# Performance work log

Measured on AMD Instinct MI355X. Metric: run time of the kernel, lower is better.

The kernel has to match this reference:

```python
import jax, jax.numpy as jnp
import numpy as np

LEAK = 0.95
THRESHOLD = 1.0
CLAMP = 3.0
LN_EPS = 1e-5


def setup_inputs() -> dict:
    key = jax.random.key(0)
    k1, k2 = jax.random.split(key)
    B, S, V, D = 8, 2048, 57344, 1536
    token_ids = jax.random.randint(k1, (B, S), 0, V, dtype=jnp.int64)
    emb_table = jax.random.normal(k2, (V, D), dtype=jnp.float32) * 0.02
    gamma = jnp.ones((D,), dtype=jnp.float32)
    beta = jnp.zeros((D,), dtype=jnp.float32)
    return {"token_ids": token_ids, "emb_table": emb_table, "gamma": gamma, "beta": beta}


def _layernorm(x, gamma, beta):
    mu = jnp.mean(x, axis=-1, keepdims=True)
    var = jnp.mean(jnp.square(x - mu), axis=-1, keepdims=True)
    return (x - mu) * jax.lax.rsqrt(var + LN_EPS) * gamma + beta


def _lif_scan(x):
    # x: [B, S, D]; sequential LIF recurrence over time axis S
    B, S, D = x.shape
    v0 = jnp.zeros((B, D), dtype=x.dtype)

    def step(v, xt):
        v = v * LEAK + xt
        v = jnp.clip(v, -CLAMP, CLAMP)
        spike = (v >= THRESHOLD).astype(x.dtype)
        return v * (1.0 - spike), spike

    _, spikes = jax.lax.scan(step, v0, jnp.swapaxes(x, 0, 1))  # spikes: [S, B, D]
    return jnp.swapaxes(spikes, 0, 1)


def reference(token_ids, emb_table, gamma, beta):
    x = emb_table[token_ids]          # [B, S, D] embedding lookup
    x = _layernorm(x, gamma, beta)    # continuous residual stream
    spikes = _lif_scan(x)             # 0/1 spike tensor [B, S, D]
    return spikes, x
```

## Files before the change

kernel.cpp:

```cpp
#include <hip/hip_runtime.h>


constexpr int Bv = 8, Sv = 2048, Dv = 1536;
constexpr int Cn = 32;
constexpr int Ln = Sv / Cn;
constexpr int Wn = 64;
constexpr int BD = Bv * Dv;
constexpr int TNMAX = Ln + Wn;

constexpr size_t FLAG_OFF  = 0;
constexpr size_t STATS_OFF = 64;
constexpr size_t SPEC0_OFF = STATS_OFF + (size_t)2 * Bv * Sv * 8;
constexpr size_t SPEC1_OFF = SPEC0_OFF + (size_t)Cn * BD * 8;
constexpr size_t WS_NEED   = SPEC1_OFF + (size_t)Cn * BD * 8;

__device__ __forceinline__ double ln_x64(float e, double mu, double rs,
                                         double gd, double bd) {
#pragma clang fp contract(off)
    return (((double)e - mu) * rs) * gd + bd;
}
__device__ __forceinline__ double lif_step(double v, double x, bool& spike) {
#pragma clang fp contract(off)
    double vv = v * 0.95;
    vv = vv + x;
    vv = fmin(fmax(vv, -3.0), 3.0);
    spike = (vv >= 1.0);
    return spike ? 0.0 : vv;
}

extern "C" __global__ __launch_bounds__(1024)
void detect_tok64(const int* __restrict__ tok, int* __restrict__ flag)
{
    __shared__ int any_nz;
    if (threadIdx.x == 0) any_nz = 0;
    __syncthreads();
    int nz = 0;
    for (int i = threadIdx.x; i < (Bv * Sv) / 2; i += 1024) nz |= tok[2 * i + 1];
    if (nz) atomicOr(&any_nz, 1);
    __syncthreads();
    if (threadIdx.x == 0) flag[0] = (any_nz == 0) ? 1 : 0;
}

extern "C" __global__ __launch_bounds__(128)
void ln_stats_kernel(const int* __restrict__ tok,
                     const float* __restrict__ emb,
                     const float* __restrict__ gamma,
                     const float* __restrict__ beta,
                     float* __restrict__ x_out,
                     double* __restrict__ stats,
                     const int* __restrict__ tok64_flag)
{
#pragma clang fp contract(off)
    __shared__ double p1[2], p2[2];

    const int row = blockIdx.x;
    const int t   = threadIdx.x;
    const int lane = t & 63, wave = t >> 6;

    const int shift = tok64_flag[0];
    const long long tk = (long long)tok[(size_t)row << shift];
    const float* src = emb + tk * (long long)Dv;

    float4 xv[3];
#pragma unroll
    for (int k = 0; k < 3; ++k) xv[k] = reinterpret_cast<const float4*>(src)[t + 128 * k];

    double s = 0.0;
#pragma unroll
    for (int k = 0; k < 3; ++k) {
        s += (double)xv[k].x; s += (double)xv[k].y;
        s += (double)xv[k].z; s += (double)xv[k].w;
    }
#pragma unroll
    for (int off = 1; off < 64; off <<= 1) s += __shfl_xor(s, off);
    if (lane == 0) p1[wave] = s;
    __syncthreads();
    const double mu = (p1[0] + p1[1]) / 1536.0;

    double q = 0.0;
#pragma unroll
    for (int k = 0; k < 3; ++k) {
        double d0 = (double)xv[k].x - mu; q += d0 * d0;
        double d1 = (double)xv[k].y - mu; q += d1 * d1;
        double d2 = (double)xv[k].z - mu; q += d2 * d2;
        double d3 = (double)xv[k].w - mu; q += d3 * d3;
    }
#pragma unroll
    for (int off = 1; off < 64; off <<= 1) q += __shfl_xor(q, off);
    if (lane == 0) p2[wave] = q;
    __syncthreads();
    const double var  = (p2[0] + p2[1]) / 1536.0;
    const double rstd = 1.0 / sqrt(var + 1e-5);

    if (t == 0) { stats[2 * row] = mu; stats[2 * row + 1] = rstd; }

    float* dst = x_out + (long long)row * Dv;
#pragma unroll
    for (int k = 0; k < 3; ++k) {
        const int f4 = t + 128 * k;
        const float4 g4 = reinterpret_cast<const float4*>(gamma)[f4];
        const float4 b4 = reinterpret_cast<const float4*>(beta)[f4];
        float4 o;
        o.x = (float)((((double)xv[k].x - mu) * rstd) * (double)g4.x + (double)b4.x);
        o.y = (float)((((double)xv[k].y - mu) * rstd) * (double)g4.y + (double)b4.y);
        o.z = (float)((((double)xv[k].z - mu) * rstd) * (double)g4.z + (double)b4.z);
        o.w = (float)((((double)xv[k].w - mu) * rstd) * (double)g4.w + (double)b4.w);
        reinterpret_cast<float4*>(dst)[f4] = o;
    }
}

extern "C" __global__ __launch_bounds__(256, 6)
void lif64_spec(const int* __restrict__ tok,
                const float* __restrict__ emb,
                const float* __restrict__ gamma,
                const float* __restrict__ beta,
                const double* __restrict__ stats,
                float* __restrict__ spk,
                double* __restrict__ spec_start,
                double* __restrict__ spec_end,
                const int* __restrict__ tok64_flag)
{
    constexpr int DBLK = Dv / 256;
    __shared__ int     tokl[TNMAX];
    __shared__ double2 statl[TNMAX];

    const int t    = threadIdx.x;
    const int bid  = blockIdx.x;
    const int dblk = bid % DBLK;
    const int c    = (bid / DBLK) % Cn;
    const int b    = bid / (DBLK * Cn);
    const int d    = dblk * 256 + t;

    const int s0 = c * Ln;
    const int sw = (c == 0) ? 0 : s0 - Wn;
    const int TN = s0 + Ln - sw;
    const int warm = s0 - sw;
    const int rowbase = b * Sv;

    if (t < TN) {
        const int row = rowbase + sw + t;
        const int shift = tok64_flag[0];
        tokl[t]  = tok[(size_t)row << shift];
        statl[t] = reinterpret_cast<const double2*>(stats)[row];
    }
    __syncthreads();

    const double gd = (double)gamma[d];
    const double bd = (double)beta[d];
    float* sp = spk + (size_t)b * Sv * Dv + d;

    constexpr int U = 16;
    float ecur[U], enxt[U];
#pragma unroll
    for (int k = 0; k < U; ++k)
        ecur[k] = emb[(long long)tokl[k] * Dv + d];

    double v = 0.0, vstart = 0.0;
    for (int i = 0; i < TN; i += U) {
        if (i + U < TN) {
#pragma unroll
            for (int k = 0; k < U; ++k)
                enxt[k] = emb[(long long)tokl[i + U + k] * Dv + d];
        }
#pragma unroll
        for (int k = 0; k < U; ++k) {
            const int idx = i + k;
            if (idx == warm) vstart = v;
            const double2 st = statl[idx];
            const double x = ln_x64(ecur[k], st.x, st.y, gd, bd);
            bool spike;
            const double vn = lif_step(v, x, spike);
            if (idx >= warm)
                __builtin_nontemporal_store(spike ? 1.0f : 0.0f,
                                            &sp[(size_t)(sw + idx) * Dv]);
            v = vn;
        }
#pragma unroll
        for (int k = 0; k < U; ++k) ecur[k] = enxt[k];
    }

    const size_t chain = (size_t)b * Dv + d;
    spec_start[(size_t)c * BD + chain] = vstart;
    spec_end[(size_t)c * BD + chain]   = v;
}

extern "C" __global__ __launch_bounds__(64)
void lif64_fixup(const int* __restrict__ tok,
                 const float* __restrict__ emb,
                 const float* __restrict__ gamma,
                 const float* __restrict__ beta,
                 const double* __restrict__ stats,
                 const double* __restrict__ spec_start,
                 const double* __restrict__ spec_end,
                 float* __restrict__ spk,
                 const int* __restrict__ tok64_flag)
{
    const int gid = blockIdx.x * 64 + threadIdx.x;
    const int b = gid / Dv;
    const int d = gid - b * Dv;
    const int shift = tok64_flag[0];
    const double gd = (double)gamma[d];
    const double bd = (double)beta[d];
    const int rowbase = b * Sv;
    float* sp = spk + (size_t)b * Sv * Dv + d;

    double v = 0.0;
    for (int c = 0; c < Cn; ++c) {
        const double vs = spec_start[(size_t)c * BD + gid];
        const double ve = spec_end[(size_t)c * BD + gid];
        if (v == vs) { v = ve; continue; }
        constexpr int U = 8;
        const int s0 = c * Ln;
        float  ecur[U], enxt[U];
        double mcur[U], mnxt[U], rcur[U], rnxt[U];
#pragma unroll
        for (int k = 0; k < U; ++k) {
            const int row = rowbase + s0 + k;
            const long long tk = (long long)tok[(size_t)row << shift];
            ecur[k] = emb[tk * (long long)Dv + d];
            mcur[k] = stats[2 * row];
            rcur[k] = stats[2 * row + 1];
        }
        for (int i = 0; i < Ln; i += U) {
            if (i + U < Ln) {
#pragma unroll
                for (int k = 0; k < U; ++k) {
                    const int row = rowbase + s0 + i + U + k;
                    const long long tk = (long long)tok[(size_t)row << shift];
                    enxt[k] = emb[tk * (long long)Dv + d];
                    mnxt[k] = stats[2 * row];
                    rnxt[k] = stats[2 * row + 1];
                }
            }
#pragma unroll
            for (int k = 0; k < U; ++k) {
                const double x = ln_x64(ecur[k], mcur[k], rcur[k], gd, bd);
                bool spike;
                v = lif_step(v, x, spike);
                sp[(size_t)(s0 + i + k) * Dv] = spike ? 1.0f : 0.0f;
            }
#pragma unroll
            for (int k = 0; k < U; ++k) {
                ecur[k] = enxt[k]; mcur[k] = mnxt[k]; rcur[k] = rnxt[k];
            }
        }
    }
}

extern "C" __global__ __launch_bounds__(64)
void lif64_seq(const int* __restrict__ tok,
               const float* __restrict__ emb,
               const float* __restrict__ gamma,
               const float* __restrict__ beta,
               const double* __restrict__ stats,
               float* __restrict__ spk,
               const int* __restrict__ tok64_flag)
{
    const int gid = blockIdx.x * 64 + threadIdx.x;
    const int b = gid / Dv;
    const int d = gid - b * Dv;
    const int shift = tok64_flag[0];
    const int rowbase = b * Sv;
    const double gd = (double)gamma[d];
    const double bd = (double)beta[d];
    float* sp = spk + (size_t)b * Sv * Dv + d;

    constexpr int U = 8;
    float  ecur[U], enxt[U];
    double mcur[U], mnxt[U], rcur[U], rnxt[U];
#pragma unroll
    for (int k = 0; k < U; ++k) {
        const int row = rowbase + k;
        const long long tk = (long long)tok[(size_t)row << shift];
        ecur[k] = emb[tk * (long long)Dv + d];
        mcur[k] = stats[2 * row];
        rcur[k] = stats[2 * row + 1];
    }
    double v = 0.0;
    for (int s = 0; s < Sv; s += U) {
        if (s + U < Sv) {
#pragma unroll
            for (int k = 0; k < U; ++k) {
                const int row = rowbase + s + U + k;
                const long long tk = (long long)tok[(size_t)row << shift];
                enxt[k] = emb[tk * (long long)Dv + d];
                mnxt[k] = stats[2 * row];
                rnxt[k] = stats[2 * row + 1];
            }
        }
#pragma unroll
        for (int k = 0; k < U; ++k) {
            const double x = ln_x64(ecur[k], mcur[k], rcur[k], gd, bd);
            bool spike;
            v = lif_step(v, x, spike);
            __builtin_nontemporal_store(spike ? 1.0f : 0.0f, &sp[(size_t)(s + k) * Dv]);
        }
#pragma unroll
        for (int k = 0; k < U; ++k) { ecur[k] = enxt[k]; mcur[k] = mnxt[k]; rcur[k] = rnxt[k]; }
    }
}

extern "C" void kernel_launch(void* const* d_in, const int* in_sizes, int n_in,
                              void* d_out, int out_size, void* d_ws, size_t ws_size,
                              hipStream_t stream)
{
    const int*   tok   = (const int*)  d_in[0];
    const float* emb   = (const float*)d_in[1];
    const float* gamma = (const float*)d_in[2];
    const float* beta  = (const float*)d_in[3];

    float* out = (float*)d_out;
    float* spk = out;
    float* x   = out + (size_t)Bv * Sv * Dv;

    int*    flg   = (int*)((char*)d_ws + FLAG_OFF);
    double* stats = (double*)((char*)d_ws + STATS_OFF);

    detect_tok64<<<1, 1024, 0, stream>>>(tok, flg);
    ln_stats_kernel<<<Bv * Sv, 128, 0, stream>>>(tok, emb, gamma, beta, x, stats, flg);

    if (ws_size >= WS_NEED) {
        double* spec0 = (double*)((char*)d_ws + SPEC0_OFF);
        double* spec1 = (double*)((char*)d_ws + SPEC1_OFF);
        lif64_spec<<<Bv * Cn * (Dv / 256), 256, 0, stream>>>(
            tok, emb, gamma, beta, stats, spk, spec0, spec1, flg);
        lif64_fixup<<<BD / 64, 64, 0, stream>>>(
            tok, emb, gamma, beta, stats, spec0, spec1, spk, flg);
    } else {
        lif64_seq<<<BD / 64, 64, 0, stream>>>(tok, emb, gamma, beta, stats, spk, flg);
    }
}
```

Measured before the change: 117.9 us.

## Process two channels per thread in LIF spec pass and skip identity gamma/beta

Each thread in the speculative LIF kernel now handles two adjacent channels, using float2 loads for embeddings and 8-byte nontemporal stores for spikes. The start and end speculation states are packed into one double2 array, so the fixup kernel reads them with a single load. A runtime check on gamma==1 and beta==0 selects a cheaper normalization path that skips the affine multiply-add. In exchange the grid has half as many blocks, so there is less parallelism to hide gather latency, and the unroll depth drops from 16 to 8.

New measurement: 131.9 us. 1.12x slower.

```diff
diff --git a/kernel.cpp b/kernel.cpp
--- a/kernel.cpp
+++ b/kernel.cpp
@@ -10,14 +10,17 @@
 
 constexpr size_t FLAG_OFF  = 0;
 constexpr size_t STATS_OFF = 64;
-constexpr size_t SPEC0_OFF = STATS_OFF + (size_t)2 * Bv * Sv * 8;
-constexpr size_t SPEC1_OFF = SPEC0_OFF + (size_t)Cn * BD * 8;
-constexpr size_t WS_NEED   = SPEC1_OFF + (size_t)Cn * BD * 8;
+constexpr size_t SE_OFF    = STATS_OFF + (size_t)2 * Bv * Sv * 8;
+constexpr size_t WS_NEED   = SE_OFF + (size_t)Cn * BD * 16;
 
 __device__ __forceinline__ double ln_x64(float e, double mu, double rs,
                                          double gd, double bd) {
 #pragma clang fp contract(off)
     return (((double)e - mu) * rs) * gd + bd;
+}
+__device__ __forceinline__ double ln_x64_triv(float e, double mu, double rs) {
+#pragma clang fp contract(off)
+    return ((double)e - mu) * rs;
 }
 __device__ __forceinline__ double lif_step(double v, double x, bool& spike) {
 #pragma clang fp contract(off)
@@ -29,16 +32,28 @@
 }
 
 extern "C" __global__ __launch_bounds__(1024)
-void detect_tok64(const int* __restrict__ tok, int* __restrict__ flag)
-{
-    __shared__ int any_nz;
-    if (threadIdx.x == 0) any_nz = 0;
+void detect_flags(const int* __restrict__ tok,
+                  const float* __restrict__ gamma,
+                  const float* __restrict__ beta,
+                  int* __restrict__ flag)
+{
+    __shared__ int any_nz, any_gb;
+    if (threadIdx.x == 0) { any_nz = 0; any_gb = 0; }
     __syncthreads();
     int nz = 0;
     for (int i = threadIdx.x; i < (Bv * Sv) / 2; i += 1024) nz |= tok[2 * i + 1];
-    if (nz) atomicOr(&any_nz, 1);
-    __syncthreads();
-    if (threadIdx.x == 0) flag[0] = (any_nz == 0) ? 1 : 0;
+    int bad = 0;
+    for (int i = threadIdx.x; i < Dv; i += 1024) {
+        bad |= (__float_as_uint(gamma[i]) != 0x3f800000u);
+        bad |= (__float_as_uint(beta[i])  != 0u);
+    }
+    if (nz)  atomicOr(&any_nz, 1);
+    if (bad) atomicOr(&any_gb, 1);
+    __syncthreads();
+    if (threadIdx.x == 0) {
+        flag[0] = (any_nz == 0) ? 1 : 0;
+        flag[1] = (any_gb == 0) ? 1 : 0;
+    }
 }
 
 extern "C" __global__ __launch_bounds__(128)
@@ -109,18 +124,79 @@
     }
 }
 
-extern "C" __global__ __launch_bounds__(256, 6)
+template<bool TRIV>
+__device__ __forceinline__ void spec_body(
+    const float* __restrict__ emb,
+    const float* __restrict__ gamma,
+    const float* __restrict__ beta,
+    const int* __restrict__ tokl,
+    const double2* __restrict__ statl,
+    int TN, int warm, int sw, int d0,
+    float* __restrict__ sp,
+    double2* __restrict__ se,
+    double& v0o, double& v1o, double& vs0o, double& vs1o)
+{
+    double gd0 = 1.0, bd0 = 0.0, gd1 = 1.0, bd1 = 0.0;
+    if (!TRIV) {
+        const float2 g2 = *reinterpret_cast<const float2*>(&gamma[d0]);
+        const float2 b2 = *reinterpret_cast<const float2*>(&beta[d0]);
+        gd0 = g2.x; gd1 = g2.y; bd0 = b2.x; bd1 = b2.y;
+    }
+    constexpr int U = 8;
+    float2 ecur[U], enxt[U];
+#pragma unroll
+    for (int k = 0; k < U; ++k)
+        ecur[k] = *reinterpret_cast<const float2*>(&emb[(long long)tokl[k] * Dv + d0]);
+
+    double v0 = 0.0, v1 = 0.0, vs0 = 0.0, vs1 = 0.0;
+    for (int i = 0; i < TN; i += U) {
+        if (i + U < TN) {
+#pragma unroll
+            for (int k = 0; k < U; ++k)
+                enxt[k] = *reinterpret_cast<const float2*>(
+                              &emb[(long long)tokl[i + U + k] * Dv + d0]);
+        }
+#pragma unroll
+        for (int k = 0; k < U; ++k) {
+            const int idx = i + k;
+            if (idx == warm) { vs0 = v0; vs1 = v1; }
+            const double2 st = statl[idx];
+            double x0, x1;
+            if (TRIV) {
+                x0 = ln_x64_triv(ecur[k].x, st.x, st.y);
+                x1 = ln_x64_triv(ecur[k].y, st.x, st.y);
+            } else {
+                x0 = ln_x64(ecur[k].x, st.x, st.y, gd0, bd0);
+                x1 = ln_x64(ecur[k].y, st.x, st.y, gd1, bd1);
+            }
+            bool s0b, s1b;
+            v0 = lif_step(v0, x0, s0b);
+            v1 = lif_step(v1, x1, s1b);
+            if (idx >= warm) {
+                union { float2 f2; double d8; } u;
+                u.f2.x = s0b ? 1.0f : 0.0f;
+                u.f2.y = s1b ? 1.0f : 0.0f;
+                __builtin_nontemporal_store(
+                    u.d8, reinterpret_cast<double*>(&sp[(size_t)(sw + idx) * Dv]));
+            }
+        }
+#pragma unroll
+        for (int k = 0; k < U; ++k) ecur[k] = enxt[k];
+    }
+    v0o = v0; v1o = v1; vs0o = vs0; vs1o = vs1;
+}
+
+extern "C" __global__ __launch_bounds__(256)
 void lif64_spec(const int* __restrict__ tok,
                 const float* __restrict__ emb,
                 const float* __restrict__ gamma,
                 const float* __restrict__ beta,
                 const double* __restrict__ stats,
                 float* __restrict__ spk,
-                double* __restrict__ spec_start,
-                double* __restrict__ spec_end,
-                const int* __restrict__ tok64_flag)
-{
-    constexpr int DBLK = Dv / 256;
+                double2* __restrict__ se,
+                const int* __restrict__ flags)
+{
+    constexpr int DBLK = Dv / 512;
     __shared__ int     tokl[TNMAX];
     __shared__ double2 statl[TNMAX];
 
@@ -129,7 +205,7 @@
     const int dblk = bid % DBLK;
     const int c    = (bid / DBLK) % Cn;
     const int b    = bid / (DBLK * Cn);
-    const int d    = dblk * 256 + t;
+    const int d0   = dblk * 512 + 2 * t;
 
     const int s0 = c * Ln;
     const int sw = (c == 0) ? 0 : s0 - Wn;
@@ -139,49 +215,27 @@
 
     if (t < TN) {
         const int row = rowbase + sw + t;
-        const int shift = tok64_flag[0];
+        const int shift = flags[0];
         tokl[t]  = tok[(size_t)row << shift];
         statl[t] = reinterpret_cast<const double2*>(stats)[row];
     }
     __syncthreads();
 
-    const double gd = (double)gamma[d];
-    const double bd = (double)beta[d];
-    float* sp = spk + (size_t)b * Sv * Dv + d;
-
-    constexpr int U = 16;
-    float ecur[U], enxt[U];
-#pragma unroll
-    for (int k = 0; k < U; ++k)
-        ecur[k] = emb[(long long)tokl[k] * Dv + d];
-
-    double v = 0.0, vstart = 0.0;
-    for (int i = 0; i < TN; i += U) {
-        if (i + U < TN) {
-#pragma unroll
-            for (int k = 0; k < U; ++k)
-                enxt[k] = emb[(long long)tokl[i + U + k] * Dv + d];
-        }
-#pragma unroll
-        for (int k = 0; k < U; ++k) {
-            const int idx = i + k;
-            if (idx == warm) vstart = v;
-            const double2 st = statl[idx];
-            const double x = ln_x64(ecur[k], st.x, st.y, gd, bd);
-            bool spike;
-            const double vn = lif_step(v, x, spike);
-            if (idx >= warm)
-                __builtin_nontemporal_store(spike ? 1.0f : 0.0f,
-                                            &sp[(size_t)(sw + idx) * Dv]);
-            v = vn;
-        }
-#pragma unroll
-        for (int k = 0; k < U; ++k) ecur[k] = enxt[k];
-    }
-
-    const size_t chain = (size_t)b * Dv + d;
-    spec_start[(size_t)c * BD + chain] = vstart;
-    spec_end[(size_t)c * BD + chain]   = v;
+    float* sp = spk + (size_t)b * Sv * Dv + d0;
+    double v0, v1, vs0, vs1;
+    if (flags[1]) {
+        spec_body<true >(emb, gamma, beta, tokl, statl, TN, warm, sw, d0, sp,
+                         se, v0, v1, vs0, vs1);
+    } else {
+        spec_body<false>(emb, gamma, beta, tokl, statl, TN, warm, sw, d0, sp,
+                         se, v0, v1, vs0, vs1);
+    }
+
+    const size_t chain0 = (size_t)b * Dv + d0;
+    double2 a; a.x = vs0; a.y = v0;
+    double2 bq; bq.x = vs1; bq.y = v1;
+    se[(size_t)c * BD + chain0]     = a;
+    se[(size_t)c * BD + chain0 + 1] = bq;
 }
 
 extern "C" __global__ __launch_bounds__(64)
@@ -190,15 +244,14 @@
                  const float* __restrict__ gamma,
                  const float* __restrict__ beta,
                  const double* __restrict__ stats,
-                 const double* __restrict__ spec_start,
-                 const double* __restrict__ spec_end,
+                 const double2* __restrict__ se,
                  float* __restrict__ spk,
-                 const int* __restrict__ tok64_flag)
+                 const int* __restrict__ flags)
 {
     const int gid = blockIdx.x * 64 + threadIdx.x;
     const int b = gid / Dv;
     const int d = gid - b * Dv;
-    const int shift = tok64_flag[0];
+    const int shift = flags[0];
     const double gd = (double)gamma[d];
     const double bd = (double)beta[d];
     const int rowbase = b * Sv;
@@ -206,9 +259,8 @@
 
     double v = 0.0;
     for (int c = 0; c < Cn; ++c) {
-        const double vs = spec_start[(size_t)c * BD + gid];
-        const double ve = spec_end[(size_t)c * BD + gid];
-        if (v == vs) { v = ve; continue; }
+        const double2 sec = se[(size_t)c * BD + gid];
+        if (v == sec.x) { v = sec.y; continue; }
         constexpr int U = 8;
         const int s0 = c * Ln;
         float  ecur[U], enxt[U];
@@ -254,12 +306,12 @@
                const float* __restrict__ beta,
                const double* __restrict__ stats,
                float* __restrict__ spk,
-               const int* __restrict__ tok64_flag)
+               const int* __restrict__ flags)
 {
     const int gid = blockIdx.x * 64 + threadIdx.x;
     const int b = gid / Dv;
     const int d = gid - b * Dv;
-    const int shift = tok64_flag[0];
+    const int shift = flags[0];
     const int rowbase = b * Sv;
     const double gd = (double)gamma[d];
     const double bd = (double)beta[d];
@@ -316,16 +368,15 @@
     int*    flg   = (int*)((char*)d_ws + FLAG_OFF);
     double* stats = (double*)((char*)d_ws + STATS_OFF);
 
-    detect_tok64<<<1, 1024, 0, stream>>>(tok, flg);
+    detect_flags<<<1, 1024, 0, stream>>>(tok, gamma, beta, flg);
     ln_stats_kernel<<<Bv * Sv, 128, 0, stream>>>(tok, emb, gamma, beta, x, stats, flg);
 
     if (ws_size >= WS_NEED) {
-        double* spec0 = (double*)((char*)d_ws + SPEC0_OFF);
-        double* spec1 = (double*)((char*)d_ws + SPEC1_OFF);
-        lif64_spec<<<Bv * Cn * (Dv / 256), 256, 0, stream>>>(
-            tok, emb, gamma, beta, stats, spk, spec0, spec1, flg);
+        double2* se = (double2*)((char*)d_ws + SE_OFF);
+        lif64_spec<<<Bv * Cn * (Dv / 512), 256, 0, stream>>>(
+            tok, emb, gamma, beta, stats, spk, se, flg);
         lif64_fixup<<<BD / 64, 64, 0, stream>>>(
-            tok, emb, gamma, beta, stats, spec0, spec1, spk, flg);
+            tok, emb, gamma, beta, stats, se, spk, flg);
     } else {
         lif64_seq<<<BD / 64, 64, 0, stream>>>(tok, emb, gamma, beta, stats, spk, flg);
     }
```

## Feed LIF kernels from stored LN output plus 16-bit residual instead of embedding gather

Applied to the files above, without the earlier changes.

The layernorm kernel now also writes a 16-bit correction term per element, so the double-precision normalized value can be rebuilt from the float output plus this short. The speculative and fixup LIF kernels then stream the stored x and correction contiguously instead of gathering embedding rows by token and recomputing layernorm from per-row stats. The per-chunk start and end voltages are packed into one double2, and the fixup kernel prefetches them four chunks ahead. This adds 2 bytes per element of extra writes and reads plus a larger workspace, in exchange for sequential, likely cache-resident reads. The fallback path writes the correction array over the stats region, which looks unsafe.

Measured after the change: 151.2 us. 28.3% more time.

```diff
diff --git a/kernel.cpp b/kernel.cpp
--- a/kernel.cpp
+++ b/kernel.cpp
@@ -6,19 +6,13 @@
 constexpr int Ln = Sv / Cn;
 constexpr int Wn = 64;
 constexpr int BD = Bv * Dv;
-constexpr int TNMAX = Ln + Wn;
 
 constexpr size_t FLAG_OFF  = 0;
 constexpr size_t STATS_OFF = 64;
-constexpr size_t SPEC0_OFF = STATS_OFF + (size_t)2 * Bv * Sv * 8;
-constexpr size_t SPEC1_OFF = SPEC0_OFF + (size_t)Cn * BD * 8;
-constexpr size_t WS_NEED   = SPEC1_OFF + (size_t)Cn * BD * 8;
-
-__device__ __forceinline__ double ln_x64(float e, double mu, double rs,
-                                         double gd, double bd) {
-#pragma clang fp contract(off)
-    return (((double)e - mu) * rs) * gd + bd;
-}
+constexpr size_t SE_OFF    = STATS_OFF + (size_t)2 * Bv * Sv * 8;
+constexpr size_t LO_OFF    = SE_OFF + (size_t)Cn * BD * 16;
+constexpr size_t WS_NEED   = LO_OFF + (size_t)Bv * Sv * Dv * 2;
+
 __device__ __forceinline__ double lif_step(double v, double x, bool& spike) {
 #pragma clang fp contract(off)
     double vv = v * 0.95;
@@ -26,6 +20,29 @@
     vv = fmin(fmax(vv, -3.0), 3.0);
     spike = (vv >= 1.0);
     return spike ? 0.0 : vv;
+}
+__device__ __forceinline__ double ln_x64(float e, double mu, double rs,
+                                         double gd, double bd) {
+#pragma clang fp contract(off)
+    return (((double)e - mu) * rs) * gd + bd;
+}
+
+__device__ __forceinline__ short encode_lo(double x64, float hi) {
+    unsigned u = __float_as_uint(hi);
+    unsigned e = (u >> 23) & 0xFFu;
+    if (e <= 23u) return 0;
+    const double inv_ulp = (double)__uint_as_float((277u - e) << 23);
+    double s = (x64 - (double)hi) * inv_ulp * 65536.0;
+    int q = __double2int_rn(s);
+    q = (q > 32767) ? 32767 : q;
+    return (short)q;
+}
+__device__ __forceinline__ double decode_x(float hi, short q) {
+    unsigned u = __float_as_uint(hi);
+    unsigned e = (u >> 23) & 0xFFu;
+    unsigned ef = (e > 24u) ? (e - 23u) : 1u;
+    const double ulp = (double)__uint_as_float(ef << 23);
+    return (double)hi + (double)q * (ulp * (1.0 / 65536.0));
 }
 
 extern "C" __global__ __launch_bounds__(1024)
@@ -47,6 +64,7 @@
                      const float* __restrict__ gamma,
                      const float* __restrict__ beta,
                      float* __restrict__ x_out,
+                     short* __restrict__ lo_out,
                      double* __restrict__ stats,
                      const int* __restrict__ tok64_flag)
 {
@@ -94,36 +112,33 @@
 
     if (t == 0) { stats[2 * row] = mu; stats[2 * row + 1] = rstd; }
 
-    float* dst = x_out + (long long)row * Dv;
+    float* dst = x_out  + (long long)row * Dv;
+    short* dlo = lo_out + (long long)row * Dv;
 #pragma unroll
     for (int k = 0; k < 3; ++k) {
         const int f4 = t + 128 * k;
         const float4 g4 = reinterpret_cast<const float4*>(gamma)[f4];
         const float4 b4 = reinterpret_cast<const float4*>(beta)[f4];
-        float4 o;
-        o.x = (float)((((double)xv[k].x - mu) * rstd) * (double)g4.x + (double)b4.x);
-        o.y = (float)((((double)xv[k].y - mu) * rstd) * (double)g4.y + (double)b4.y);
-        o.z = (float)((((double)xv[k].z - mu) * rstd) * (double)g4.z + (double)b4.z);
-        o.w = (float)((((double)xv[k].w - mu) * rstd) * (double)g4.w + (double)b4.w);
+        const double x0 = (((double)xv[k].x - mu) * rstd) * (double)g4.x + (double)b4.x;
+        const double x1 = (((double)xv[k].y - mu) * rstd) * (double)g4.y + (double)b4.y;
+        const double x2 = (((double)xv[k].z - mu) * rstd) * (double)g4.z + (double)b4.z;
+        const double x3 = (((double)xv[k].w - mu) * rstd) * (double)g4.w + (double)b4.w;
+        float4 o; o.x = (float)x0; o.y = (float)x1; o.z = (float)x2; o.w = (float)x3;
+        short4 lo4;
+        lo4.x = encode_lo(x0, o.x); lo4.y = encode_lo(x1, o.y);
+        lo4.z = encode_lo(x2, o.z); lo4.w = encode_lo(x3, o.w);
         reinterpret_cast<float4*>(dst)[f4] = o;
-    }
-}
-
-extern "C" __global__ __launch_bounds__(256, 6)
-void lif64_spec(const int* __restrict__ tok,
-                const float* __restrict__ emb,
-                const float* __restrict__ gamma,
-                const float* __restrict__ beta,
-                const double* __restrict__ stats,
+        reinterpret_cast<short4*>(dlo)[f4] = lo4;
+    }
+}
+
+extern "C" __global__ __launch_bounds__(256)
+void lif64_spec(const float* __restrict__ xs,
+                const short* __restrict__ lo,
                 float* __restrict__ spk,
-                double* __restrict__ spec_start,
-                double* __restrict__ spec_end,
-                const int* __restrict__ tok64_flag)
+                double2* __restrict__ se)
 {
     constexpr int DBLK = Dv / 256;
-    __shared__ int     tokl[TNMAX];
-    __shared__ double2 statl[TNMAX];
-
     const int t    = threadIdx.x;
     const int bid  = blockIdx.x;
     const int dblk = bid % DBLK;
@@ -135,115 +150,108 @@
     const int sw = (c == 0) ? 0 : s0 - Wn;
     const int TN = s0 + Ln - sw;
     const int warm = s0 - sw;
-    const int rowbase = b * Sv;
-
-    if (t < TN) {
-        const int row = rowbase + sw + t;
-        const int shift = tok64_flag[0];
-        tokl[t]  = tok[(size_t)row << shift];
-        statl[t] = reinterpret_cast<const double2*>(stats)[row];
-    }
-    __syncthreads();
-
-    const double gd = (double)gamma[d];
-    const double bd = (double)beta[d];
-    float* sp = spk + (size_t)b * Sv * Dv + d;
-
-    constexpr int U = 16;
-    float ecur[U], enxt[U];
-#pragma unroll
-    for (int k = 0; k < U; ++k)
-        ecur[k] = emb[(long long)tokl[k] * Dv + d];
+
+    const size_t base = ((size_t)b * Sv + sw) * (size_t)Dv + d;
+    const float* xp = xs  + base;
+    const short* lp = lo  + base;
+    float*       sp = spk + base;
+
+    constexpr int U = 8;
+    float h0[U], h1[U]; short q0[U], q1[U];
+#pragma unroll
+    for (int k = 0; k < U; ++k) { h0[k] = xp[k * Dv]; q0[k] = lp[k * Dv]; }
 
     double v = 0.0, vstart = 0.0;
     for (int i = 0; i < TN; i += U) {
         if (i + U < TN) {
 #pragma unroll
-            for (int k = 0; k < U; ++k)
-                enxt[k] = emb[(long long)tokl[i + U + k] * Dv + d];
+            for (int k = 0; k < U; ++k) {
+                h1[k] = xp[(i + U + k) * Dv];
+                q1[k] = lp[(i + U + k) * Dv];
+            }
         }
 #pragma unroll
         for (int k = 0; k < U; ++k) {
             const int idx = i + k;
             if (idx == warm) vstart = v;
-            const double2 st = statl[idx];
-            const double x = ln_x64(ecur[k], st.x, st.y, gd, bd);
+            const double x = decode_x(h0[k], q0[k]);
             bool spike;
-            const double vn = lif_step(v, x, spike);
+            v = lif_step(v, x, spike);
             if (idx >= warm)
                 __builtin_nontemporal_store(spike ? 1.0f : 0.0f,
-                                            &sp[(size_t)(sw + idx) * Dv]);
-            v = vn;
-        }
-#pragma unroll
-        for (int k = 0; k < U; ++k) ecur[k] = enxt[k];
+                                            &sp[(size_t)idx * Dv]);
+        }
+#pragma unroll
+        for (int k = 0; k < U; ++k) { h0[k] = h1[k]; q0[k] = q1[k]; }
     }
 
     const size_t chain = (size_t)b * Dv + d;
-    spec_start[(size_t)c * BD + chain] = vstart;
-    spec_end[(size_t)c * BD + chain]   = v;
+    double2 a; a.x = vstart; a.y = v;
+    se[(size_t)c * BD + chain] = a;
+}
+
+__device__ __forceinline__ double fix_chunk(const float* __restrict__ xp,
+                                            const short* __restrict__ lp,
+                                            float* __restrict__ sp, double v)
+{
+    constexpr int U = 8;
+    float h0[U], h1[U]; short q0[U], q1[U];
+#pragma unroll
+    for (int k = 0; k < U; ++k) { h0[k] = xp[k * Dv]; q0[k] = lp[k * Dv]; }
+    for (int i = 0; i < Ln; i += U) {
+        if (i + U < Ln) {
+#pragma unroll
+            for (int k = 0; k < U; ++k) {
+                h1[k] = xp[(i + U + k) * Dv];
+                q1[k] = lp[(i + U + k) * Dv];
+            }
+        }
+#pragma unroll
+        for (int k = 0; k < U; ++k) {
+            const double x = decode_x(h0[k], q0[k]);
+            bool spike;
+            v = lif_step(v, x, spike);
+            sp[(size_t)(i + k) * Dv] = spike ? 1.0f : 0.0f;
+        }
+#pragma unroll
+        for (int k = 0; k < U; ++k) { h0[k] = h1[k]; q0[k] = q1[k]; }
+    }
+    return v;
 }
 
 extern "C" __global__ __launch_bounds__(64)
-void lif64_fixup(const int* __restrict__ tok,
-                 const float* __restrict__ emb,
-                 const float* __restrict__ gamma,
-                 const float* __restrict__ beta,
-                 const double* __restrict__ stats,
-                 const double* __restrict__ spec_start,
-                 const double* __restrict__ spec_end,
-                 float* __restrict__ spk,
-                 const int* __restrict__ tok64_flag)
+void lif64_fixup(const float* __restrict__ xs,
+                 const short* __restrict__ lo,
+                 const double2* __restrict__ se,
+                 float* __restrict__ spk)
 {
     const int gid = blockIdx.x * 64 + threadIdx.x;
     const int b = gid / Dv;
     const int d = gid - b * Dv;
-    const int shift = tok64_flag[0];
-    const double gd = (double)gamma[d];
-    const double bd = (double)beta[d];
-    const int rowbase = b * Sv;
-    float* sp = spk + (size_t)b * Sv * Dv + d;
+    const size_t cb = (size_t)b * Sv * Dv + d;
+
+    double2 buf[4], nbuf[4];
+#pragma unroll
+    for (int j = 0; j < 4; ++j) buf[j] = se[(size_t)j * BD + gid];
 
     double v = 0.0;
-    for (int c = 0; c < Cn; ++c) {
-        const double vs = spec_start[(size_t)c * BD + gid];
-        const double ve = spec_end[(size_t)c * BD + gid];
-        if (v == vs) { v = ve; continue; }
-        constexpr int U = 8;
-        const int s0 = c * Ln;
-        float  ecur[U], enxt[U];
-        double mcur[U], mnxt[U], rcur[U], rnxt[U];
-#pragma unroll
-        for (int k = 0; k < U; ++k) {
-            const int row = rowbase + s0 + k;
-            const long long tk = (long long)tok[(size_t)row << shift];
-            ecur[k] = emb[tk * (long long)Dv + d];
-            mcur[k] = stats[2 * row];
-            rcur[k] = stats[2 * row + 1];
-        }
-        for (int i = 0; i < Ln; i += U) {
-            if (i + U < Ln) {
-#pragma unroll
-                for (int k = 0; k < U; ++k) {
-                    const int row = rowbase + s0 + i + U + k;
-                    const long long tk = (long long)tok[(size_t)row << shift];
-                    enxt[k] = emb[tk * (long long)Dv + d];
-                    mnxt[k] = stats[2 * row];
-                    rnxt[k] = stats[2 * row + 1];
-                }
+    for (int c4 = 0; c4 < Cn; c4 += 4) {
+        if (c4 + 4 < Cn) {
+#pragma unroll
+            for (int j = 0; j < 4; ++j)
+                nbuf[j] = se[(size_t)(c4 + 4 + j) * BD + gid];
+        }
+#pragma unroll
+        for (int j = 0; j < 4; ++j) {
+            const int c = c4 + j;
+            if (v == buf[j].x) { v = buf[j].y; }
+            else {
+                const size_t off = cb + (size_t)(c * Ln) * Dv;
+                v = fix_chunk(xs + off, lo + off, spk + off, v);
             }
-#pragma unroll
-            for (int k = 0; k < U; ++k) {
-                const double x = ln_x64(ecur[k], mcur[k], rcur[k], gd, bd);
-                bool spike;
-                v = lif_step(v, x, spike);
-                sp[(size_t)(s0 + i + k) * Dv] = spike ? 1.0f : 0.0f;
-            }
-#pragma unroll
-            for (int k = 0; k < U; ++k) {
-                ecur[k] = enxt[k]; mcur[k] = mnxt[k]; rcur[k] = rnxt[k];
-            }
-        }
+        }
+#pragma unroll
+        for (int j = 0; j < 4; ++j) buf[j] = nbuf[j];
     }
 }
 
@@ -254,12 +262,12 @@
                const float* __restrict__ beta,
                const double* __restrict__ stats,
                float* __restrict__ spk,
-               const int* __restrict__ tok64_flag)
+               const int* __restrict__ flags)
 {
     const int gid = blockIdx.x * 64 + threadIdx.x;
     const int b = gid / Dv;
     const int d = gid - b * Dv;
-    const int shift = tok64_flag[0];
+    const int shift = flags[0];
     const int rowbase = b * Sv;
     const double gd = (double)gamma[d];
     const double bd = (double)beta[d];
@@ -317,16 +325,18 @@
     double* stats = (double*)((char*)d_ws + STATS_OFF);
 
     detect_tok64<<<1, 1024, 0, stream>>>(tok, flg);
-    ln_stats_kernel<<<Bv * Sv, 128, 0, stream>>>(tok, emb, gamma, beta, x, stats, flg);
 
     if (ws_size >= WS_NEED) {
-        double* spec0 = (double*)((char*)d_ws + SPEC0_OFF);
-        double* spec1 = (double*)((char*)d_ws + SPEC1_OFF);
-        lif64_spec<<<Bv * Cn * (Dv / 256), 256, 0, stream>>>(
-            tok, emb, gamma, beta, stats, spk, spec0, spec1, flg);
-        lif64_fixup<<<BD / 64, 64, 0, stream>>>(
-            tok, emb, gamma, beta, stats, spec0, spec1, spk, flg);
+        double2* se  = (double2*)((char*)d_ws + SE_OFF);
+        short*   lo  = (short*)((char*)d_ws + LO_OFF);
+        ln_stats_kernel<<<Bv * Sv, 128, 0, stream>>>(
+            tok, emb, gamma, beta, x, lo, stats, flg);
+        lif64_spec<<<Bv * Cn * (Dv / 256), 256, 0, stream>>>(x, lo, spk, se);
+        lif64_fixup<<<BD / 64, 64, 0, stream>>>(x, lo, se, spk);
     } else {
+        short* lo_dummy = (short*)((char*)d_ws + STATS_OFF);
+        ln_stats_kernel<<<Bv * Sv, 128, 0, stream>>>(
+            tok, emb, gamma, beta, x, lo_dummy, stats, flg);
         lif64_seq<<<BD / 64, 64, 0, stream>>>(tok, emb, gamma, beta, stats, spk, flg);
     }
 }
```

## Move normalized output write into LIF scan kernel and pack speculative state

Applied to the files above, without the earlier changes.

The stats kernel no longer writes the layernormed x tensor. Instead, the speculative LIF scan and the sequential fallback store x as they compute it, which removes a separate full write pass from the stats kernel. The start and end speculative states are packed into one double2 array, and the fixup kernel prefetches them four chunks ahead so the convergence checks do not stall on memory. The spec kernel now does more stores per step and its unroll drops from 16 to 8 with the occupancy hint removed, which may change latency hiding and register use.

New measurement: 133.6 us. 1.13x slower.

```diff
diff --git a/kernel.cpp b/kernel.cpp
--- a/kernel.cpp
+++ b/kernel.cpp
@@ -10,9 +10,8 @@
 
 constexpr size_t FLAG_OFF  = 0;
 constexpr size_t STATS_OFF = 64;
-constexpr size_t SPEC0_OFF = STATS_OFF + (size_t)2 * Bv * Sv * 8;
-constexpr size_t SPEC1_OFF = SPEC0_OFF + (size_t)Cn * BD * 8;
-constexpr size_t WS_NEED   = SPEC1_OFF + (size_t)Cn * BD * 8;
+constexpr size_t SE_OFF    = STATS_OFF + (size_t)2 * Bv * Sv * 8;
+constexpr size_t WS_NEED   = SE_OFF + (size_t)Cn * BD * 16;
 
 __device__ __forceinline__ double ln_x64(float e, double mu, double rs,
                                          double gd, double bd) {
@@ -44,9 +43,6 @@
 extern "C" __global__ __launch_bounds__(128)
 void ln_stats_kernel(const int* __restrict__ tok,
                      const float* __restrict__ emb,
-                     const float* __restrict__ gamma,
-                     const float* __restrict__ beta,
-                     float* __restrict__ x_out,
                      double* __restrict__ stats,
                      const int* __restrict__ tok64_flag)
 {
@@ -93,31 +89,17 @@
     const double rstd = 1.0 / sqrt(var + 1e-5);
 
     if (t == 0) { stats[2 * row] = mu; stats[2 * row + 1] = rstd; }
-
-    float* dst = x_out + (long long)row * Dv;
-#pragma unroll
-    for (int k = 0; k < 3; ++k) {
-        const int f4 = t + 128 * k;
-        const float4 g4 = reinterpret_cast<const float4*>(gamma)[f4];
-        const float4 b4 = reinterpret_cast<const float4*>(beta)[f4];
-        float4 o;
-        o.x = (float)((((double)xv[k].x - mu) * rstd) * (double)g4.x + (double)b4.x);
-        o.y = (float)((((double)xv[k].y - mu) * rstd) * (double)g4.y + (double)b4.y);
-        o.z = (float)((((double)xv[k].z - mu) * rstd) * (double)g4.z + (double)b4.z);
-        o.w = (float)((((double)xv[k].w - mu) * rstd) * (double)g4.w + (double)b4.w);
-        reinterpret_cast<float4*>(dst)[f4] = o;
-    }
-}
-
-extern "C" __global__ __launch_bounds__(256, 6)
+}
+
+extern "C" __global__ __launch_bounds__(256)
 void lif64_spec(const int* __restrict__ tok,
                 const float* __restrict__ emb,
                 const float* __restrict__ gamma,
                 const float* __restrict__ beta,
                 const double* __restrict__ stats,
+                float* __restrict__ x_out,
                 float* __restrict__ spk,
-                double* __restrict__ spec_start,
-                double* __restrict__ spec_end,
+                double2* __restrict__ se,
                 const int* __restrict__ tok64_flag)
 {
     constexpr int DBLK = Dv / 256;
@@ -147,9 +129,10 @@
 
     const double gd = (double)gamma[d];
     const double bd = (double)beta[d];
-    float* sp = spk + (size_t)b * Sv * Dv + d;
-
-    constexpr int U = 16;
+    float* sp = spk   + (size_t)b * Sv * Dv + d;
+    float* xo = x_out + (size_t)b * Sv * Dv + d;
+
+    constexpr int U = 8;
     float ecur[U], enxt[U];
 #pragma unroll
     for (int k = 0; k < U; ++k)
@@ -170,9 +153,11 @@
             const double x = ln_x64(ecur[k], st.x, st.y, gd, bd);
             bool spike;
             const double vn = lif_step(v, x, spike);
-            if (idx >= warm)
-                __builtin_nontemporal_store(spike ? 1.0f : 0.0f,
-                                            &sp[(size_t)(sw + idx) * Dv]);
+            if (idx >= warm) {
+                const size_t off = (size_t)(sw + idx) * Dv;
+                __builtin_nontemporal_store((float)x, &xo[off]);
+                __builtin_nontemporal_store(spike ? 1.0f : 0.0f, &sp[off]);
+            }
             v = vn;
         }
 #pragma unroll
@@ -180,8 +165,8 @@
     }
 
     const size_t chain = (size_t)b * Dv + d;
-    spec_start[(size_t)c * BD + chain] = vstart;
-    spec_end[(size_t)c * BD + chain]   = v;
+    double2 a; a.x = vstart; a.y = v;
+    se[(size_t)c * BD + chain] = a;
 }
 
 extern "C" __global__ __launch_bounds__(64)
@@ -190,8 +175,7 @@
                  const float* __restrict__ gamma,
                  const float* __restrict__ beta,
                  const double* __restrict__ stats,
-                 const double* __restrict__ spec_start,
-                 const double* __restrict__ spec_end,
+                 const double2* __restrict__ se,
                  float* __restrict__ spk,
                  const int* __restrict__ tok64_flag)
 {
@@ -204,46 +188,59 @@
     const int rowbase = b * Sv;
     float* sp = spk + (size_t)b * Sv * Dv + d;
 
+    double2 buf[4], nbuf[4];
+#pragma unroll
+    for (int j = 0; j < 4; ++j) buf[j] = se[(size_t)j * BD + gid];
+
     double v = 0.0;
-    for (int c = 0; c < Cn; ++c) {
-        const double vs = spec_start[(size_t)c * BD + gid];
-        const double ve = spec_end[(size_t)c * BD + gid];
-        if (v == vs) { v = ve; continue; }
-        constexpr int U = 8;
-        const int s0 = c * Ln;
-        float  ecur[U], enxt[U];
-        double mcur[U], mnxt[U], rcur[U], rnxt[U];
-#pragma unroll
-        for (int k = 0; k < U; ++k) {
-            const int row = rowbase + s0 + k;
-            const long long tk = (long long)tok[(size_t)row << shift];
-            ecur[k] = emb[tk * (long long)Dv + d];
-            mcur[k] = stats[2 * row];
-            rcur[k] = stats[2 * row + 1];
-        }
-        for (int i = 0; i < Ln; i += U) {
-            if (i + U < Ln) {
+    for (int c4 = 0; c4 < Cn; c4 += 4) {
+        if (c4 + 4 < Cn) {
+#pragma unroll
+            for (int j = 0; j < 4; ++j)
+                nbuf[j] = se[(size_t)(c4 + 4 + j) * BD + gid];
+        }
+#pragma unroll
+        for (int j = 0; j < 4; ++j) {
+            const int c = c4 + j;
+            if (v == buf[j].x) { v = buf[j].y; continue; }
+            constexpr int U = 8;
+            const int s0 = c * Ln;
+            float  ecur[U], enxt[U];
+            double mcur[U], mnxt[U], rcur[U], rnxt[U];
+#pragma unroll
+            for (int k = 0; k < U; ++k) {
+                const int row = rowbase + s0 + k;
+                const long long tk = (long long)tok[(size_t)row << shift];
+                ecur[k] = emb[tk * (long long)Dv + d];
+                mcur[k] = stats[2 * row];
+                rcur[k] = stats[2 * row + 1];
+            }
+            for (int i = 0; i < Ln; i += U) {
+                if (i + U < Ln) {
+#pragma unroll
+                    for (int k = 0; k < U; ++k) {
+                        const int row = rowbase + s0 + i + U + k;
+                        const long long tk = (long long)tok[(size_t)row << shift];
+                        enxt[k] = emb[tk * (long long)Dv + d];
+                        mnxt[k] = stats[2 * row];
+                        rnxt[k] = stats[2 * row + 1];
+                    }
+                }
 #pragma unroll
                 for (int k = 0; k < U; ++k) {
-                    const int row = rowbase + s0 + i + U + k;
-                    const long long tk = (long long)tok[(size_t)row << shift];
-                    enxt[k] = emb[tk * (long long)Dv + d];
-                    mnxt[k] = stats[2 * row];
-                    rnxt[k] = stats[2 * row + 1];
+                    const double x = ln_x64(ecur[k], mcur[k], rcur[k], gd, bd);
+                    bool spike;
+                    v = lif_step(v, x, spike);
+                    sp[(size_t)(s0 + i + k) * Dv] = spike ? 1.0f : 0.0f;
+                }
+#pragma unroll
+                for (int k = 0; k < U; ++k) {
+                    ecur[k] = enxt[k]; mcur[k] = mnxt[k]; rcur[k] = rnxt[k];
                 }
             }
-#pragma unroll
-            for (int k = 0; k < U; ++k) {
-                const double x = ln_x64(ecur[k], mcur[k], rcur[k], gd, bd);
-                bool spike;
-                v = lif_step(v, x, spike);
-                sp[(size_t)(s0 + i + k) * Dv] = spike ? 1.0f : 0.0f;
-            }
-#pragma unroll
-            for (int k = 0; k < U; ++k) {
-                ecur[k] = enxt[k]; mcur[k] = mnxt[k]; rcur[k] = rnxt[k];
-            }
-        }
+        }
+#pragma unroll
+        for (int j = 0; j < 4; ++j) buf[j] = nbuf[j];
     }
 }
 
@@ -253,17 +250,19 @@
                const float* __restrict__ gamma,
                const float* __restrict__ beta,
                const double* __restrict__ stats,
+               float* __restrict__ x_out,
                float* __restrict__ spk,
-               const int* __restrict__ tok64_flag)
+               const int* __restrict__ flags)
 {
     const int gid = blockIdx.x * 64 + threadIdx.x;
     const int b = gid / Dv;
     const int d = gid - b * Dv;
-    const int shift = tok64_flag[0];
+    const int shift = flags[0];
     const int rowbase = b * Sv;
     const double gd = (double)gamma[d];
     const double bd = (double)beta[d];
-    float* sp = spk + (size_t)b * Sv * Dv + d;
+    float* sp = spk   + (size_t)b * Sv * Dv + d;
+    float* xo = x_out + (size_t)b * Sv * Dv + d;
 
     constexpr int U = 8;
     float  ecur[U], enxt[U];
@@ -293,7 +292,9 @@
             const double x = ln_x64(ecur[k], mcur[k], rcur[k], gd, bd);
             bool spike;
             v = lif_step(v, x, spike);
-            __builtin_nontemporal_store(spike ? 1.0f : 0.0f, &sp[(size_t)(s + k) * Dv]);
+            const size_t off = (size_t)(s + k) * Dv;
+            __builtin_nontemporal_store((float)x, &xo[off]);
+            __builtin_nontemporal_store(spike ? 1.0f : 0.0f, &sp[off]);
         }
 #pragma unroll
         for (int k = 0; k < U; ++k) { ecur[k] = enxt[k]; mcur[k] = mnxt[k]; rcur[k] = rnxt[k]; }
@@ -317,16 +318,16 @@
     double* stats = (double*)((char*)d_ws + STATS_OFF);
 
     detect_tok64<<<1, 1024, 0, stream>>>(tok, flg);
-    ln_stats_kernel<<<Bv * Sv, 128, 0, stream>>>(tok, emb, gamma, beta, x, stats, flg);
+    ln_stats_kernel<<<Bv * Sv, 128, 0, stream>>>(tok, emb, stats, flg);
 
     if (ws_size >= WS_NEED) {
-        double* spec0 = (double*)((char*)d_ws + SPEC0_OFF);
-        double* spec1 = (double*)((char*)d_ws + SPEC1_OFF);
+        double2* se = (double2*)((char*)d_ws + SE_OFF);
         lif64_spec<<<Bv * Cn * (Dv / 256), 256, 0, stream>>>(
-            tok, emb, gamma, beta, stats, spk, spec0, spec1, flg);
+            tok, emb, gamma, beta, stats, x, spk, se, flg);
         lif64_fixup<<<BD / 64, 64, 0, stream>>>(
-            tok, emb, gamma, beta, stats, spec0, spec1, spk, flg);
+            tok, emb, gamma, beta, stats, se, spk, flg);
     } else {
-        lif64_seq<<<BD / 64, 64, 0, stream>>>(tok, emb, gamma, beta, stats, spk, flg);
-    }
-}
+        lif64_seq<<<BD / 64, 64, 0, stream>>>(
+            tok, emb, gamma, beta, stats, x, spk, flg);
+    }
+}
```
